# Kernel tuning notes

Hardware: AMD Instinct MI355X
Metric: run time of the kernel (lower is better)

The kernel has to match this reference:

```python
import jax, jax.numpy as jnp
import numpy as np


def _resize_bilinear_ac(x, Ht, Wt):
    # bilinear resize with align_corners=True; x: [B,C,h,w] -> [B,C,Ht,Wt]
    B, C, h, w = x.shape
    ys = jnp.linspace(0.0, h - 1.0, Ht)
    xs = jnp.linspace(0.0, w - 1.0, Wt)
    y0 = jnp.floor(ys).astype(jnp.int32)
    y1 = jnp.minimum(y0 + 1, h - 1)
    x0 = jnp.floor(xs).astype(jnp.int32)
    x1 = jnp.minimum(x0 + 1, w - 1)
    wy = (ys - y0).astype(x.dtype)[None, None, :, None]
    wx = (xs - x0).astype(x.dtype)[None, None, None, :]
    r0 = x[:, :, y0, :]
    r1 = x[:, :, y1, :]
    v00 = r0[:, :, :, x0]; v01 = r0[:, :, :, x1]
    v10 = r1[:, :, :, x0]; v11 = r1[:, :, :, x1]
    return (1 - wy) * ((1 - wx) * v00 + wx * v01) + wy * ((1 - wx) * v10 + wx * v11)


def _grid_sample_zeros_ac(img, grid):
    # F.grid_sample(mode='bilinear', padding_mode='zeros', align_corners=True)
    # img: [B,C,H,W], grid: [B,H,W,2] in [-1,1] (x, y)
    B, C, H, W = img.shape
    x = (grid[..., 0] + 1.0) * 0.5 * (W - 1)  # [B,H,W] pixel coords
    y = (grid[..., 1] + 1.0) * 0.5 * (H - 1)
    x0 = jnp.floor(x)
    y0 = jnp.floor(y)
    wx = (x - x0)[:, None]  # [B,1,H,W]
    wy = (y - y0)[:, None]

    def gather(xi, yi):
        valid = ((xi >= 0) & (xi <= W - 1) & (yi >= 0) & (yi <= H - 1)).astype(img.dtype)
        xc = jnp.clip(xi, 0, W - 1).astype(jnp.int32)
        yc = jnp.clip(yi, 0, H - 1).astype(jnp.int32)
        v = jax.vmap(lambda im, yy, xx: im[:, yy, xx])(img, yc, xc)  # [B,C,H,W]
        return v * valid[:, None]

    v00 = gather(x0, y0)
    v01 = gather(x0 + 1, y0)
    v10 = gather(x0, y0 + 1)
    v11 = gather(x0 + 1, y0 + 1)
    return (1 - wy) * ((1 - wx) * v00 + wx * v01) + wy * ((1 - wx) * v10 + wx * v11)


def setup_inputs() -> dict:
    key = jax.random.key(0)
    k1, k2, k3 = jax.random.split(key, 3)
    B, C, H, W = 8, 3, 384, 1280
    h, w = 96, 320
    image = jax.random.normal(k1, (B, C, H, W), dtype=jnp.float32)
    # positive disparity (fraction of width, scaled by W inside forward)
    disp = jax.random.uniform(k2, (B, 1, h, w), dtype=jnp.float32, minval=0.01, maxval=0.3)
    scene = jax.random.normal(k3, (B, 3, h, w), dtype=jnp.float32) * 0.1
    K = jnp.array([[371.0, 0.0, 320.0], [0.0, 371.0, 96.0], [0.0, 0.0, 1.0]], dtype=jnp.float32)
    intrinsic = jnp.tile(K[None], (B, 1, 1))
    aug_size = jnp.tile(jnp.array([192.0, 640.0], dtype=jnp.float32)[None], (B, 1))
    return {"image": image, "disp": disp, "scene": scene, "intrinsic": intrinsic, "aug_size": aug_size}


def reference(image, disp, scene, intrinsic, aug_size):
    B, C, H, W = image.shape
    # interpolate_as(disp, image) * W
    disp_full = _resize_bilinear_ac(disp, H, W) * W
    # rel_scale = local_scale / aug_size, local_scale = (H, W)
    rel = jnp.array([H, W], dtype=aug_size.dtype) / aug_size  # [B,2] = (sy, sx)
    sy, sx = rel[:, 0], rel[:, 1]
    fx = intrinsic[:, 0, 0] * sx
    fy = intrinsic[:, 1, 1] * sy
    cx = intrinsic[:, 0, 2] * sx
    cy = intrinsic[:, 1, 2] * sy
    z = jnp.zeros_like(fx)
    o = jnp.ones_like(fx)
    K = jnp.stack([jnp.stack([fx, z, cx], 1),
                   jnp.stack([z, fy, cy], 1),
                   jnp.stack([z, z, o], 1)], 1)  # [B,3,3]
    # disp2depth_stereo_clamp
    depth = jnp.clip(fx[:, None, None, None] * 0.54 / (disp_full + 1e-8), 0.001, 80.0)
    # pixel2point
    xg, yg = jnp.meshgrid(jnp.arange(W, dtype=jnp.float32), jnp.arange(H, dtype=jnp.float32))  # [H,W]
    pix = jnp.stack([xg.ravel(), yg.ravel(), jnp.ones(H * W, dtype=jnp.float32)], 0)  # [3,HW]
    Kinv = jnp.linalg.inv(K)
    point = jnp.einsum('bij,jn->bin', Kinv, pix) * depth.reshape(B, 1, -1)  # [B,3,HW]
    # point2pixel_ms
    scene_full = _resize_bilinear_ac(scene, H, W)
    point_form = point.reshape(B, 3, H, W) + scene_full
    proj = jnp.einsum('bij,bjn->bin', K, point_form.reshape(B, 3, -1))
    coord = (proj[:, 0:2] / (proj[:, 2:3] + 1e-8)).reshape(B, 2, H, W)
    nx = coord[:, 0] / (W - 1) * 2.0 - 1.0
    ny = coord[:, 1] / (H - 1) * 2.0 - 1.0
    grid = jnp.stack([nx, ny], -1)  # [B,H,W,2]
    return _grid_sample_zeros_ac(image, grid)
```

## Files before the change

kernel.cpp:

```cpp
#include <hip/hip_runtime.h>
#include <hip/hip_fp16.h>

#define BATCH 8
#define CH 3
#define H_OUT 384
#define W_OUT 1280
#define H_IN 96
#define W_IN 320
#define HW_OUT (H_OUT * W_OUT)
#define HW_IN (H_IN * W_IN)

#define XS_PER_ROW 20
#define YSEGS (H_OUT / 4)
#define CHUNKS_PER_B (YSEGS * XS_PER_ROW)

#define LCOLS 18
#define LROWS 3

#define P1STRIDE 1282
#define P1_HALVES ((size_t)(1 + (size_t)BATCH * H_OUT * P1STRIDE) * 4)
#define P1_BYTES (P1_HALVES * 2)

struct __attribute__((packed, aligned(4))) f2 { float x, y; };
struct __attribute__((packed, aligned(8))) h8 { unsigned int w[4]; };
struct __attribute__((packed, aligned(8))) u4 { unsigned int w[4]; };

typedef float vf4 __attribute__((ext_vector_type(4)));

static __device__ __forceinline__ __half2 u2h2(unsigned int u) {
    return *reinterpret_cast<__half2*>(&u);
}
static __device__ __forceinline__ unsigned int h2u(__half2 h) {
    return *reinterpret_cast<unsigned int*>(&h);
}

__global__ __launch_bounds__(256) void pack_single_kernel(
    const float* __restrict__ image, __half* __restrict__ pk)
{
    int bid = blockIdx.x;
    int b = bid & 7;
    int chunk = bid >> 3;
    int p = chunk * 1024 + threadIdx.x * 4;
    int y = p / W_OUT;
    int x = p - y * W_OUT;

    const float* ib = image + (size_t)b * (CH * HW_OUT) + p;
    vf4 A  = __builtin_nontemporal_load(reinterpret_cast<const vf4*>(ib));
    vf4 Bv = __builtin_nontemporal_load(reinterpret_cast<const vf4*>(ib + HW_OUT));
    vf4 Cv = __builtin_nontemporal_load(reinterpret_cast<const vf4*>(ib + 2 * HW_OUT));

    u4 s0, s1;
    s0.w[0] = h2u(__floats2half2_rn(A.x, Bv.x));
    s0.w[1] = h2u(__floats2half2_rn(Cv.x, 0.0f));
    s0.w[2] = h2u(__floats2half2_rn(A.y, Bv.y));
    s0.w[3] = h2u(__floats2half2_rn(Cv.y, 0.0f));
    s1.w[0] = h2u(__floats2half2_rn(A.z, Bv.z));
    s1.w[1] = h2u(__floats2half2_rn(Cv.z, 0.0f));
    s1.w[2] = h2u(__floats2half2_rn(A.w, Bv.w));
    s1.w[3] = h2u(__floats2half2_rn(Cv.w, 0.0f));

    __half* pd = pk + 4;
    size_t off = ((size_t)(b * H_OUT + y) * P1STRIDE + x) * 4;
    *reinterpret_cast<u4*>(pd + off) = s0;
    *reinterpret_cast<u4*>(pd + off + 8) = s1;

    int gt = bid * 256 + threadIdx.x;
    if (gt < BATCH * H_OUT) {
        uint2 z; z.x = 0u; z.y = 0u;
        size_t r = (size_t)gt;
        *reinterpret_cast<uint2*>(pd + (r * P1STRIDE + 1280) * 4) = z;
        *reinterpret_cast<uint2*>(pd + (r * P1STRIDE + 1281) * 4) = z;
        if (gt == 0) *reinterpret_cast<uint2*>(pk) = z;
    }
}

template <int MODE>
__global__ __launch_bounds__(256) void warp_sceneflow_kernel(
    const float* __restrict__ image,
    const __half* __restrict__ pk,
    const float* __restrict__ disp,
    const float* __restrict__ scene,
    const float* __restrict__ intrin,
    const float* __restrict__ aug,
    float* __restrict__ out)
{
    int bid = blockIdx.x;
    int b = bid & 7;
    int c = bid >> 3;
    int ys = c / XS_PER_ROW;
    int xs = c - ys * XS_PER_ROW;
    int ybase = ys * 4;
    int xbase = xs * 64;

    int tid = threadIdx.x;
    int wave = tid >> 6;
    int lane = tid & 63;
    int lx16 = lane & 15;
    int ly4  = lane >> 4;
    int x = xbase + wave * 16 + lx16;
    int y = ybase + ly4;

    __shared__ float4 lds4[LROWS][LCOLS];
    int ylo = (int)((float)ybase * ((float)(H_IN - 1) / (float)(H_OUT - 1)));
    int xlo = (int)((float)xbase * ((float)(W_IN - 1) / (float)(W_OUT - 1)));
    if (tid < LROWS * LCOLS) {
        int row = tid / LCOLS;
        int col = tid - row * LCOLS;
        int gy = min(ylo + row, H_IN - 1);
        int gx = min(xlo + col, W_IN - 1);
        int gi = gy * W_IN + gx;
        const float* dp = disp + b * HW_IN;
        const float* sp = scene + b * (CH * HW_IN);
        float4 v;
        v.x = dp[gi];
        v.y = sp[gi];
        v.z = sp[HW_IN + gi];
        v.w = sp[2 * HW_IN + gi];
        lds4[row][col] = v;
    }
    __syncthreads();

    float syr = (float)H_OUT / aug[b * 2 + 0];
    float sxr = (float)W_OUT / aug[b * 2 + 1];
    float fx = intrin[b * 9 + 0] * sxr;
    float fy = intrin[b * 9 + 4] * syr;
    float cx = intrin[b * 9 + 2] * sxr;
    float cy = intrin[b * 9 + 5] * syr;
    float inv_fx = 1.0f / fx;
    float inv_fy = 1.0f / fy;

    float xsrc = (float)x * ((float)(W_IN - 1) / (float)(W_OUT - 1));
    int x0 = (int)xsrc;
    float wx = xsrc - (float)x0;
    int lx = x0 - xlo;

    float ysrc = (float)y * ((float)(H_IN - 1) / (float)(H_OUT - 1));
    int y0 = (int)ysrc;
    float wy = ysrc - (float)y0;
    int ly = y0 - ylo;

    float4 t00 = lds4[ly][lx];
    float4 t01 = lds4[ly][lx + 1];
    float4 t10 = lds4[ly + 1][lx];
    float4 t11 = lds4[ly + 1][lx + 1];

    float w00 = (1.0f - wy) * (1.0f - wx);
    float w01 = (1.0f - wy) * wx;
    float w10 = wy * (1.0f - wx);
    float w11 = wy * wx;

    float dval = w00 * t00.x + w01 * t01.x + w10 * t10.x + w11 * t11.x;
    float sc0  = w00 * t00.y + w01 * t01.y + w10 * t10.y + w11 * t11.y;
    float sc1  = w00 * t00.z + w01 * t01.z + w10 * t10.z + w11 * t11.z;
    float sc2  = w00 * t00.w + w01 * t01.w + w10 * t10.w + w11 * t11.w;

    float disp_full = dval * (float)W_OUT;
    float depth = fminf(fmaxf(fx * 0.54f / (disp_full + 1e-8f), 0.001f), 80.0f);

    float X = ((float)x - cx) * inv_fx * depth + sc0;
    float Y = ((float)y - cy) * inv_fy * depth + sc1;
    float Z = depth + sc2;
    float u = fx * X + cx * Z;
    float v = fy * Y + cy * Z;
    float rw = 1.0f / (Z + 1e-8f);
    float gx = u * rw;
    float gy = v * rw;

    int ix0 = __float2int_rd(gx);
    int iy0 = __float2int_rd(gy);
    float fwx = gx - (float)ix0;
    float fwy = gy - (float)iy0;
    int ix1 = ix0 + 1, iy1 = iy0 + 1;
    bool vx0 = (ix0 >= 0) && (ix0 <= W_OUT - 1);
    bool vx1 = (ix1 >= 0) && (ix1 <= W_OUT - 1);
    bool vy0 = (iy0 >= 0) && (iy0 <= H_OUT - 1);
    bool vy1 = (iy1 >= 0) && (iy1 <= H_OUT - 1);
    float g00 = (1.0f - fwy) * (1.0f - fwx) * ((vx0 && vy0) ? 1.0f : 0.0f);
    float g01 = (1.0f - fwy) * fwx * ((vx1 && vy0) ? 1.0f : 0.0f);
    float g10 = fwy * (1.0f - fwx) * ((vx0 && vy1) ? 1.0f : 0.0f);
    float g11 = fwy * fwx * ((vx1 && vy1) ? 1.0f : 0.0f);
    int cy0 = min(max(iy0, 0), H_OUT - 1);
    int cy1 = min(max(iy1, 0), H_OUT - 1);

    float r0, r1, r2;
    if constexpr (MODE == 1) {
        int bx = min(max(ix0, -1), W_OUT - 1);
        const __half* pd = pk + 4;
        size_t rb0 = ((size_t)(b * H_OUT + cy0) * P1STRIDE + bx);
        size_t rb1 = ((size_t)(b * H_OUT + cy1) * P1STRIDE + bx);
        h8 L0 = *reinterpret_cast<const h8*>(pd + rb0 * 4);
        h8 L1 = *reinterpret_cast<const h8*>(pd + rb1 * 4);
        __half2 h0a = u2h2(L0.w[0]), h0b = u2h2(L0.w[1]);
        __half2 h1a = u2h2(L0.w[2]), h1b = u2h2(L0.w[3]);
        __half2 k0a = u2h2(L1.w[0]), k0b = u2h2(L1.w[1]);
        __half2 k1a = u2h2(L1.w[2]), k1b = u2h2(L1.w[3]);
        r0 = g00 * __low2float(h0a) + g01 * __low2float(h1a)
           + g10 * __low2float(k0a) + g11 * __low2float(k1a);
        r1 = g00 * __high2float(h0a) + g01 * __high2float(h1a)
           + g10 * __high2float(k0a) + g11 * __high2float(k1a);
        r2 = g00 * __low2float(h0b) + g01 * __low2float(h1b)
           + g10 * __low2float(k0b) + g11 * __low2float(k1b);
    } else {
        int cx0 = min(max(ix0, 0), W_OUT - 1);
        int cx1 = min(max(ix1, 0), W_OUT - 1);
        int xbi = min(cx0, W_OUT - 2);
        bool rcf = (cx0 != xbi);
        bool lcf = (cx1 == xbi);
        int rb0 = cy0 * W_OUT + xbi;
        int rb1 = cy1 * W_OUT + xbi;
        const float* ib = image + (size_t)b * (CH * HW_OUT);
        const float* im0 = ib;
        const float* im1 = ib + HW_OUT;
        const float* im2 = ib + 2 * HW_OUT;
        f2 P0 = *(const f2*)(im0 + rb0); f2 P1 = *(const f2*)(im0 + rb1);
        f2 Q0 = *(const f2*)(im1 + rb0); f2 Q1 = *(const f2*)(im1 + rb1);
        f2 T0 = *(const f2*)(im2 + rb0); f2 T1 = *(const f2*)(im2 + rb1);
        float p00 = rcf ? P0.y : P0.x, p01 = lcf ? P0.x : P0.y;
        float p10 = rcf ? P1.y : P1.x, p11 = lcf ? P1.x : P1.y;
        float q00 = rcf ? Q0.y : Q0.x, q01 = lcf ? Q0.x : Q0.y;
        float q10 = rcf ? Q1.y : Q1.x, q11 = lcf ? Q1.x : Q1.y;
        float t00f = rcf ? T0.y : T0.x, t01f = lcf ? T0.x : T0.y;
        float t10f = rcf ? T1.y : T1.x, t11f = lcf ? T1.x : T1.y;
        r0 = g00 * p00 + g01 * p01 + g10 * p10 + g11 * p11;
        r1 = g00 * q00 + g01 * q01 + g10 * q10 + g11 * q11;
        r2 = g00 * t00f + g01 * t01f + g10 * t10f + g11 * t11f;
    }

    float* ob = out + (size_t)b * (CH * HW_OUT);
    int op = y * W_OUT + x;
    __builtin_nontemporal_store(r0, ob + op);
    __builtin_nontemporal_store(r1, ob + HW_OUT + op);
    __builtin_nontemporal_store(r2, ob + 2 * HW_OUT + op);
}

extern "C" void kernel_launch(void* const* d_in, const int* in_sizes, int n_in,
                              void* d_out, int out_size, void* d_ws, size_t ws_size,
                              hipStream_t stream) {
    const float* image  = (const float*)d_in[0];
    const float* disp   = (const float*)d_in[1];
    const float* scene  = (const float*)d_in[2];
    const float* intrin = (const float*)d_in[3];
    const float* aug    = (const float*)d_in[4];
    float* out = (float*)d_out;

    const int grid = BATCH * CHUNKS_PER_B;

    if (ws_size >= P1_BYTES) {
        __half* pk = (__half*)d_ws;
        pack_single_kernel<<<BATCH * HW_OUT / 1024, 256, 0, stream>>>(image, pk);
        warp_sceneflow_kernel<1><<<grid, 256, 0, stream>>>(
            image, pk, disp, scene, intrin, aug, out);
    } else {
        warp_sceneflow_kernel<0><<<grid, 256, 0, stream>>>(
            image, nullptr, disp, scene, intrin, aug, out);
    }
}
```

Before: 52.83 us.

## Pack image rows in interleaved pairs for the fp16 gather layout

The prepack kernel now interleaves two consecutive image rows per 16-byte entry, so each column entry holds RGB for rows 2k and 2k+1. The sampler reads four 8-byte half-precision texels from the pair layout instead of two 16-byte horizontal pairs. The aim is better cache-line locality for vertically adjacent taps, at the cost of four loads instead of two, which may not help when cy0 and cy1 fall in different pairs. The workspace footprint is unchanged apart from padding.

```diff
diff --git a/kernel.cpp b/kernel.cpp
--- a/kernel.cpp
+++ b/kernel.cpp
@@ -17,12 +17,12 @@
 #define LCOLS 18
 #define LROWS 3
 
-#define P1STRIDE 1282
-#define P1_HALVES ((size_t)(1 + (size_t)BATCH * H_OUT * P1STRIDE) * 4)
-#define P1_BYTES (P1_HALVES * 2)
+#define NPAIR (H_OUT / 2)
+#define PSTRIDE 1282
+#define PK_ENTRIES ((size_t)BATCH * NPAIR * PSTRIDE)
+#define PK_BYTES (PK_ENTRIES * 16)
 
 struct __attribute__((packed, aligned(4))) f2 { float x, y; };
-struct __attribute__((packed, aligned(8))) h8 { unsigned int w[4]; };
 struct __attribute__((packed, aligned(8))) u4 { unsigned int w[4]; };
 
 typedef float vf4 __attribute__((ext_vector_type(4)));
@@ -34,43 +34,54 @@
     return *reinterpret_cast<unsigned int*>(&h);
 }
 
-__global__ __launch_bounds__(256) void pack_single_kernel(
+__global__ __launch_bounds__(256) void pack_pair_kernel(
     const float* __restrict__ image, __half* __restrict__ pk)
 {
     int bid = blockIdx.x;
     int b = bid & 7;
     int chunk = bid >> 3;
-    int p = chunk * 1024 + threadIdx.x * 4;
-    int y = p / W_OUT;
-    int x = p - y * W_OUT;
-
-    const float* ib = image + (size_t)b * (CH * HW_OUT) + p;
-    vf4 A  = __builtin_nontemporal_load(reinterpret_cast<const vf4*>(ib));
-    vf4 Bv = __builtin_nontemporal_load(reinterpret_cast<const vf4*>(ib + HW_OUT));
-    vf4 Cv = __builtin_nontemporal_load(reinterpret_cast<const vf4*>(ib + 2 * HW_OUT));
-
-    u4 s0, s1;
-    s0.w[0] = h2u(__floats2half2_rn(A.x, Bv.x));
-    s0.w[1] = h2u(__floats2half2_rn(Cv.x, 0.0f));
-    s0.w[2] = h2u(__floats2half2_rn(A.y, Bv.y));
-    s0.w[3] = h2u(__floats2half2_rn(Cv.y, 0.0f));
-    s1.w[0] = h2u(__floats2half2_rn(A.z, Bv.z));
-    s1.w[1] = h2u(__floats2half2_rn(Cv.z, 0.0f));
-    s1.w[2] = h2u(__floats2half2_rn(A.w, Bv.w));
-    s1.w[3] = h2u(__floats2half2_rn(Cv.w, 0.0f));
-
-    __half* pd = pk + 4;
-    size_t off = ((size_t)(b * H_OUT + y) * P1STRIDE + x) * 4;
-    *reinterpret_cast<u4*>(pd + off) = s0;
-    *reinterpret_cast<u4*>(pd + off + 8) = s1;
+    int q = chunk * 256 + threadIdx.x;
+    int k = q / 320;
+    int xq = (q - k * 320) * 4;
+
+    const float* r0 = image + (size_t)b * (CH * HW_OUT) + (2 * k) * W_OUT + xq;
+    const float* r1 = r0 + W_OUT;
+    vf4 A0 = __builtin_nontemporal_load(reinterpret_cast<const vf4*>(r0));
+    vf4 B0 = __builtin_nontemporal_load(reinterpret_cast<const vf4*>(r0 + HW_OUT));
+    vf4 C0 = __builtin_nontemporal_load(reinterpret_cast<const vf4*>(r0 + 2 * HW_OUT));
+    vf4 A1 = __builtin_nontemporal_load(reinterpret_cast<const vf4*>(r1));
+    vf4 B1 = __builtin_nontemporal_load(reinterpret_cast<const vf4*>(r1 + HW_OUT));
+    vf4 C1 = __builtin_nontemporal_load(reinterpret_cast<const vf4*>(r1 + 2 * HW_OUT));
+
+    size_t e0 = ((size_t)(b * NPAIR + k) * PSTRIDE + (xq + 1));
+    u4 e;
+    e.w[0] = h2u(__floats2half2_rn(A0.x, B0.x));
+    e.w[1] = h2u(__floats2half2_rn(C0.x, 0.0f));
+    e.w[2] = h2u(__floats2half2_rn(A1.x, B1.x));
+    e.w[3] = h2u(__floats2half2_rn(C1.x, 0.0f));
+    *reinterpret_cast<u4*>(pk + e0 * 8) = e;
+    e.w[0] = h2u(__floats2half2_rn(A0.y, B0.y));
+    e.w[1] = h2u(__floats2half2_rn(C0.y, 0.0f));
+    e.w[2] = h2u(__floats2half2_rn(A1.y, B1.y));
+    e.w[3] = h2u(__floats2half2_rn(C1.y, 0.0f));
+    *reinterpret_cast<u4*>(pk + (e0 + 1) * 8) = e;
+    e.w[0] = h2u(__floats2half2_rn(A0.z, B0.z));
+    e.w[1] = h2u(__floats2half2_rn(C0.z, 0.0f));
+    e.w[2] = h2u(__floats2half2_rn(A1.z, B1.z));
+    e.w[3] = h2u(__floats2half2_rn(C1.z, 0.0f));
+    *reinterpret_cast<u4*>(pk + (e0 + 2) * 8) = e;
+    e.w[0] = h2u(__floats2half2_rn(A0.w, B0.w));
+    e.w[1] = h2u(__floats2half2_rn(C0.w, 0.0f));
+    e.w[2] = h2u(__floats2half2_rn(A1.w, B1.w));
+    e.w[3] = h2u(__floats2half2_rn(C1.w, 0.0f));
+    *reinterpret_cast<u4*>(pk + (e0 + 3) * 8) = e;
 
     int gt = bid * 256 + threadIdx.x;
-    if (gt < BATCH * H_OUT) {
-        uint2 z; z.x = 0u; z.y = 0u;
-        size_t r = (size_t)gt;
-        *reinterpret_cast<uint2*>(pd + (r * P1STRIDE + 1280) * 4) = z;
-        *reinterpret_cast<uint2*>(pd + (r * P1STRIDE + 1281) * 4) = z;
-        if (gt == 0) *reinterpret_cast<uint2*>(pk) = z;
+    if (gt < BATCH * NPAIR) {
+        u4 z; z.w[0] = 0u; z.w[1] = 0u; z.w[2] = 0u; z.w[3] = 0u;
+        size_t base = (size_t)gt * PSTRIDE;
+        *reinterpret_cast<u4*>(pk + base * 8) = z;
+        *reinterpret_cast<u4*>(pk + (base + 1281) * 8) = z;
     }
 }
 
@@ -95,10 +106,8 @@
     int tid = threadIdx.x;
     int wave = tid >> 6;
     int lane = tid & 63;
-    int lx16 = lane & 15;
-    int ly4  = lane >> 4;
-    int x = xbase + wave * 16 + lx16;
-    int y = ybase + ly4;
+    int x = xbase + wave * 16 + (lane & 15);
+    int y = ybase + (lane >> 4);
 
     __shared__ float4 lds4[LROWS][LCOLS];
     int ylo = (int)((float)ybase * ((float)(H_IN - 1) / (float)(H_OUT - 1)));
@@ -184,22 +193,26 @@
 
     float r0, r1, r2;
     if constexpr (MODE == 1) {
-        int bx = min(max(ix0, -1), W_OUT - 1);
-        const __half* pd = pk + 4;
-        size_t rb0 = ((size_t)(b * H_OUT + cy0) * P1STRIDE + bx);
-        size_t rb1 = ((size_t)(b * H_OUT + cy1) * P1STRIDE + bx);
-        h8 L0 = *reinterpret_cast<const h8*>(pd + rb0 * 4);
-        h8 L1 = *reinterpret_cast<const h8*>(pd + rb1 * 4);
-        __half2 h0a = u2h2(L0.w[0]), h0b = u2h2(L0.w[1]);
-        __half2 h1a = u2h2(L0.w[2]), h1b = u2h2(L0.w[3]);
-        __half2 k0a = u2h2(L1.w[0]), k0b = u2h2(L1.w[1]);
-        __half2 k1a = u2h2(L1.w[2]), k1b = u2h2(L1.w[3]);
-        r0 = g00 * __low2float(h0a) + g01 * __low2float(h1a)
-           + g10 * __low2float(k0a) + g11 * __low2float(k1a);
-        r1 = g00 * __high2float(h0a) + g01 * __high2float(h1a)
-           + g10 * __high2float(k0a) + g11 * __high2float(k1a);
-        r2 = g00 * __low2float(h0b) + g01 * __low2float(h1b)
-           + g10 * __low2float(k0b) + g11 * __low2float(k1b);
+        int bxc = min(max(ix0, -1), W_OUT - 1);
+        int cxi = bxc + 1;
+        int pr0 = cy0 >> 1, p0 = cy0 & 1;
+        int pr1 = cy1 >> 1, p1 = cy1 & 1;
+        size_t h00 = ((size_t)(b * NPAIR + pr0) * PSTRIDE + cxi) * 8 + p0 * 4;
+        size_t h10 = ((size_t)(b * NPAIR + pr1) * PSTRIDE + cxi) * 8 + p1 * 4;
+        uint2 L00 = *reinterpret_cast<const uint2*>(pk + h00);
+        uint2 L01 = *reinterpret_cast<const uint2*>(pk + h00 + 8);
+        uint2 L10 = *reinterpret_cast<const uint2*>(pk + h10);
+        uint2 L11 = *reinterpret_cast<const uint2*>(pk + h10 + 8);
+        __half2 a00 = u2h2(L00.x), b00h = u2h2(L00.y);
+        __half2 a01 = u2h2(L01.x), b01h = u2h2(L01.y);
+        __half2 a10 = u2h2(L10.x), b10h = u2h2(L10.y);
+        __half2 a11 = u2h2(L11.x), b11h = u2h2(L11.y);
+        r0 = g00 * __low2float(a00) + g01 * __low2float(a01)
+           + g10 * __low2float(a10) + g11 * __low2float(a11);
+        r1 = g00 * __high2float(a00) + g01 * __high2float(a01)
+           + g10 * __high2float(a10) + g11 * __high2float(a11);
+        r2 = g00 * __low2float(b00h) + g01 * __low2float(b01h)
+           + g10 * __low2float(b10h) + g11 * __low2float(b11h);
     } else {
         int cx0 = min(max(ix0, 0), W_OUT - 1);
         int cx1 = min(max(ix1, 0), W_OUT - 1);
@@ -245,9 +258,9 @@
 
     const int grid = BATCH * CHUNKS_PER_B;
 
-    if (ws_size >= P1_BYTES) {
+    if (ws_size >= PK_BYTES) {
         __half* pk = (__half*)d_ws;
-        pack_single_kernel<<<BATCH * HW_OUT / 1024, 256, 0, stream>>>(image, pk);
+        pack_pair_kernel<<<BATCH * 240, 256, 0, stream>>>(image, pk);
         warp_sceneflow_kernel<1><<<grid, 256, 0, stream>>>(
             image, pk, disp, scene, intrin, aug, out);
     } else {
```

Result: slower. 62.06 us (+17.5%).
